# Kernel optimization log

Hardware: AMD Instinct MI355X
Metric: run time of the kernel (lower is better)

Reference implementation:

```python
import jax, jax.numpy as jnp
import numpy as np

T, B, D, H, Q = 512, 256, 128, 128, 8


def _qgate(z, theta):
    """Analytic simulation of the QGate circuit.

    Circuit: start |0..0>, RX(z_j) then trainable RX(theta_j) on each wire j
    (RX(a)RX(b)=RX(a+b)), then a CNOT ring w->(w+1)%Q, then <Z_w> on each wire.
    RX(phi)|0> gives <Z>=cos(phi) and independent wires; the CNOT ring permutes
    computational basis states so bit_w = XOR_{j<=w} a_j for w>=1 and
    bit_0 = XOR_{j>=1} a_j, hence <Z_w> = prod_{j<=w} cos(phi_j) for w>=1 and
    <Z_0> = prod_{j>=1} cos(phi_j). Exact, no 2^Q statevector needed.
    """
    c = jnp.cos(z + theta)                      # (B, Q)
    cp = jnp.cumprod(c, axis=-1)                # (B, Q)
    z0 = jnp.prod(c[:, 1:], axis=-1, keepdims=True)
    return jnp.concatenate([z0, cp[:, 1:]], axis=-1)


def setup_inputs() -> dict:
    key = jax.random.key(0)
    ks = jax.random.split(key, 25)
    inp = {"inputs": jax.random.normal(ks[0], (T, B, D), dtype=jnp.float32)}
    s_in = 1.0 / np.sqrt(D + H)
    s_q = 1.0 / np.sqrt(Q)
    names = ["f", "i", "g", "o"]
    for n, gname in enumerate(names):
        k = ks[1 + 6 * n: 1 + 6 * (n + 1)]
        inp["W" + gname] = jax.random.uniform(k[0], (Q, D + H), jnp.float32, -s_in, s_in)
        inp["b" + gname] = jax.random.uniform(k[1], (Q,), jnp.float32, -s_in, s_in)
        inp["th" + gname] = jax.random.normal(k[2], (Q,), jnp.float32)  # trainable RX angles
        inp["U" + gname] = jax.random.uniform(k[3], (H, Q), jnp.float32, -s_q, s_q)
        inp["c" + gname] = jax.random.uniform(k[4], (H,), jnp.float32, -s_q, s_q)
    return inp


def reference(inputs, Wf, bf, thf, Uf, cf,
              Wi, bi, thi, Ui, ci,
              Wg, bg, thg, Ug, cg,
              Wo, bo, tho, Uo, co):
    bsz = inputs.shape[1]
    hdim = Uf.shape[0]
    h0 = jnp.zeros((bsz, hdim), inputs.dtype)
    c0 = jnp.zeros((bsz, hdim), inputs.dtype)

    def gate(comb, W, b, th, U, cb):
        return _qgate(comb @ W.T + b, th) @ U.T + cb

    def step(carry, x):
        hx, cx = carry
        comb = jnp.concatenate([x, hx], axis=1)          # (B, D+H)
        f = jax.nn.sigmoid(gate(comb, Wf, bf, thf, Uf, cf))
        i = jax.nn.sigmoid(gate(comb, Wi, bi, thi, Ui, ci))
        g = jnp.tanh(gate(comb, Wg, bg, thg, Ug, cg))
        o = jax.nn.sigmoid(gate(comb, Wo, bo, tho, Uo, co))
        cx = f * cx + i * g
        hx = o * jnp.tanh(cx)
        return (hx, cx), hx

    (hx, cx), outs = jax.lax.scan(step, (h0, c0), inputs)
    return outs, hx, cx
```

## Files before the change

### kernel.cpp

```cpp
#include <hip/hip_runtime.h>

#define TT 512
#define BB 256
#define DD 128
#define HH 128
#define QQ 8

struct Params {
    const float* x;
    const float* W[4];
    const float* b[4];
    const float* th[4];
    const float* U[4];
    const float* cb[4];
    float* out;
};

__device__ __forceinline__ float rcp_f(float x)  { return __builtin_amdgcn_rcpf(x); }
__device__ __forceinline__ float exp2_f(float x) { return __builtin_amdgcn_exp2f(x); }

template<int CTRL>
__device__ __forceinline__ float dpp_mov(float x) {
    int r = __builtin_amdgcn_update_dpp(0, __float_as_int(x), CTRL, 0xF, 0xF, true);
    return __int_as_float(r);
}
template<int CTRL, int RM>
__device__ __forceinline__ float dpp_mul1(float x) {
    int r = __builtin_amdgcn_update_dpp(0x3f800000 , __float_as_int(x),
                                        CTRL, RM, 0xF, false);
    return __int_as_float(r);
}
#define RDLANE(v, l) __int_as_float(__builtin_amdgcn_readlane(__float_as_int(v), (l)))

__device__ __forceinline__ void bar_lds() {
    asm volatile("s_waitcnt lgkmcnt(0)\n\ts_barrier" ::: "memory");
}

__global__ __launch_bounds__(256, 1) void qlstm(Params p) {
    __shared__ __align__(16) float xbuf[2][8][144];
    __shared__ __align__(16) float hbuf[144];
    __shared__ float pre[512];
    __shared__ float zxbuf[2][32];

    const int tid = threadIdx.x;
    const int bId = blockIdx.x;
    const int ln  = tid & 63;
    const int wv  = tid >> 6;
    const int qub = ln >> 3;
    const int part8 = ln & 7;

    float Wh[16];
    {
        const float* Wg = p.W[wv] + qub * (DD + HH) + DD + part8 * 16;
        #pragma unroll
        for (int j = 0; j < 16; ++j) Wh[j] = Wg[j];
    }
    const float breg = p.b[wv][qub] + p.th[wv][qub];

    const int gz = 2 * (wv - 2) + (ln >> 5);
    const int qz = (ln >> 2) & 7;
    const int pz = ln & 3;
    float Wx[32];
    if (wv >= 2) {
        const float* Wg = p.W[gz] + qz * (DD + HH) + pz * 32;
        #pragma unroll
        for (int j = 0; j < 32; ++j) Wx[j] = Wg[j];
    }

    const float esc = (wv == 2) ? 2.885390081777927f : -1.442695040888963f;
    float Ua[8], Ub[8];
    #pragma unroll
    for (int j = 0; j < 8; ++j) {
        Ua[j] = p.U[wv][ln * QQ + j] * esc;
        Ub[j] = p.U[wv][(ln + 64) * QQ + j] * esc;
    }
    const float cba = p.cb[wv][ln] * esc;
    const float cbb = p.cb[wv][ln + 64] * esc;

    float cst = 0.f;
    float hn_last = 0.f;

    if (tid < 128) hbuf[tid + 4 * (tid >> 5)] = 0.f;

    const int xc_col  = (ln & 31) * 4;
    const int xc_half = ln >> 5;
    const int xc_slot = xc_col + 4 * (xc_col >> 5);
    float4 xr[4];
    #pragma unroll
    for (int j = 0; j < 4; ++j) xr[j] = make_float4(0.f, 0.f, 0.f, 0.f);

    if (wv == 3) {
        #pragma unroll
        for (int j = 0; j < 4; ++j) {
            const int row = 2 * j + xc_half;
            float4 v = *(const float4*)(p.x + ((size_t)row * BB + bId) * DD + xc_col);
            *(float4*)&xbuf[0][row][xc_slot] = v;
        }
    }
    __syncthreads();

    if (wv >= 2) {
        const float* xrow = &xbuf[0][0][36 * pz];
        float b0 = 0.f, b1 = 0.f, b2 = 0.f, b3 = 0.f;
        #pragma unroll
        for (int i = 0; i < 8; ++i) {
            float4 c4 = *(const float4*)(xrow + 4 * i);
            b0 = fmaf(Wx[4*i+0], c4.x, b0);
            b1 = fmaf(Wx[4*i+1], c4.y, b1);
            b2 = fmaf(Wx[4*i+2], c4.z, b2);
            b3 = fmaf(Wx[4*i+3], c4.w, b3);
        }
        float zx2 = (b0 + b1) + (b2 + b3);
        zx2 += dpp_mov<0xB1>(zx2);
        zx2 += dpp_mov<0x4E>(zx2);
        if ((ln & 3) == 0) zxbuf[0][8 * gz + qz] = zx2;
    }
    __syncthreads();

    const float* hsrc = &hbuf[16 * part8 + 4 * (part8 >> 1)];
    const size_t orow_step = (size_t)BB * HH;
    size_t orow = (size_t)bId * HH + tid;

    #pragma unroll 8
    for (int t = 0; t < TT; ++t) {
        const float zxs = zxbuf[t & 1][8 * wv + qub];
        const float4 h0 = ((const float4*)hsrc)[0];
        const float4 h1 = *(const float4*)(hsrc + 4);
        const float4 h2 = *(const float4*)(hsrc + 8);
        const float4 h3 = *(const float4*)(hsrc + 12);

        if (((t & 7) == 0) && wv == 3) {
            const int tch = (t >> 3) + 1;
            if (tch < TT / 8) {
                #pragma unroll
                for (int j = 0; j < 4; ++j) {
                    const int row = tch * 8 + 2 * j + xc_half;
                    xr[j] = *(const float4*)(p.x + ((size_t)row * BB + bId) * DD + xc_col);
                }
            }
        }

        float a0 = Wh[0] * h0.x, a1 = Wh[1] * h0.y, a2 = Wh[2] * h0.z, a3 = Wh[3] * h0.w;
        a0 = fmaf(Wh[4],  h1.x, a0); a1 = fmaf(Wh[5],  h1.y, a1);
        a2 = fmaf(Wh[6],  h1.z, a2); a3 = fmaf(Wh[7],  h1.w, a3);
        a0 = fmaf(Wh[8],  h2.x, a0); a1 = fmaf(Wh[9],  h2.y, a1);
        a2 = fmaf(Wh[10], h2.z, a2); a3 = fmaf(Wh[11], h2.w, a3);
        a0 = fmaf(Wh[12], h3.x, a0); a1 = fmaf(Wh[13], h3.y, a1);
        a2 = fmaf(Wh[14], h3.z, a2); a3 = fmaf(Wh[15], h3.w, a3);
        float acc = (a0 + a1) + (a2 + a3);
        acc += dpp_mov<0xB1>(acc);
        acc += dpp_mov<0x4E>(acc);
        acc += dpp_mov<0x141>(acc);
        acc += zxs + breg;

        const float cv = __cosf(acc);
        float v = cv;
        v *= dpp_mul1<0x118, 0xF>(v);
        v *= dpp_mul1<0x142, 0xA>(v);
        v *= dpp_mul1<0x143, 0xC>(v);
        float u = (ln < 8) ? 1.f : cv;
        u *= dpp_mul1<0x118, 0xF>(u);
        u *= dpp_mul1<0x142, 0xA>(u);
        u *= dpp_mul1<0x143, 0xC>(u);
        const float q0 = RDLANE(u, 63);
        const float q1 = RDLANE(v, 8);
        const float q2 = RDLANE(v, 16);
        const float q3 = RDLANE(v, 24);
        const float q4 = RDLANE(v, 32);
        const float q5 = RDLANE(v, 40);
        const float q6 = RDLANE(v, 48);
        const float q7 = RDLANE(v, 56);

        float a01 = fmaf(Ua[1], q1, Ua[0] * q0);
        float b01 = fmaf(Ub[1], q1, Ub[0] * q0);
        float a23 = fmaf(Ua[3], q3, Ua[2] * q2);
        float b23 = fmaf(Ub[3], q3, Ub[2] * q2);
        float a45 = fmaf(Ua[5], q5, Ua[4] * q4);
        float b45 = fmaf(Ub[5], q5, Ub[4] * q4);
        float a67 = fmaf(Ua[7], q7, Ua[6] * q6);
        float b67 = fmaf(Ub[7], q7, Ub[6] * q6);
        float pa = ((a01 + a23) + (a45 + a67)) + cba;
        float pb = ((b01 + b23) + (b45 + b67)) + cbb;
        pre[wv * 128 + ln]      = pa;
        pre[wv * 128 + 64 + ln] = pb;

        bar_lds();

        if (tid < 128) {
            float p_f = (wv == 0) ? pa : pre[tid];
            float p_i = (wv == 1) ? pb : pre[128 + tid];
            float p_g = pre[256 + tid];
            float p_o = pre[384 + tid];
            float fg = rcp_f(1.f + exp2_f(p_f));
            float ig = rcp_f(1.f + exp2_f(p_i));
            float gg = fmaf(-2.f, rcp_f(1.f + exp2_f(p_g)), 1.f);
            float og = rcp_f(1.f + exp2_f(p_o));
            cst = fmaf(fg, cst, ig * gg);
            float tc = fmaf(-2.f, rcp_f(1.f + exp2_f(cst * 2.885390081777927f)), 1.f);
            float hn = og * tc;
            hn_last = hn;
            hbuf[tid + 4 * (tid >> 5)] = hn;
            p.out[orow] = hn;
            orow += orow_step;
        } else {
            if (wv == 3 && (t & 7) == 6) {
                const int tch = (t >> 3) + 1;
                if (tch < TT / 8) {
                    #pragma unroll
                    for (int j = 0; j < 4; ++j) {
                        const int row = 2 * j + xc_half;
                        *(float4*)&xbuf[tch & 1][row][xc_slot] = xr[j];
                    }
                }
            }
            if (t < TT - 1) {
                const int tn = t + 1;
                const float* xrow = &xbuf[(tn >> 3) & 1][tn & 7][36 * pz];
                float4 c[8];
                #pragma unroll
                for (int i = 0; i < 8; ++i) c[i] = *(const float4*)(xrow + 4 * i);
                float b0 = Wx[0] * c[0].x, b1 = Wx[1] * c[0].y;
                float b2 = Wx[2] * c[0].z, b3 = Wx[3] * c[0].w;
                #pragma unroll
                for (int i = 1; i < 8; ++i) {
                    b0 = fmaf(Wx[4*i+0], c[i].x, b0);
                    b1 = fmaf(Wx[4*i+1], c[i].y, b1);
                    b2 = fmaf(Wx[4*i+2], c[i].z, b2);
                    b3 = fmaf(Wx[4*i+3], c[i].w, b3);
                }
                float zx2 = (b0 + b1) + (b2 + b3);
                zx2 += dpp_mov<0xB1>(zx2);
                zx2 += dpp_mov<0x4E>(zx2);
                if ((ln & 3) == 0) zxbuf[tn & 1][8 * gz + qz] = zx2;
            }
        }
        bar_lds();
    }

    if (tid < 128) {
        p.out[(size_t)TT * BB * HH + (size_t)bId * HH + tid] = hn_last;
        p.out[(size_t)TT * BB * HH + (size_t)BB * HH + (size_t)bId * HH + tid] = cst;
    }
}

extern "C" void kernel_launch(void* const* d_in, const int* in_sizes, int n_in,
                              void* d_out, int out_size, void* d_ws, size_t ws_size,
                              hipStream_t stream) {
    (void)in_sizes; (void)n_in; (void)out_size; (void)d_ws; (void)ws_size;
    Params p;
    p.x = (const float*)d_in[0];
    for (int g = 0; g < 4; ++g) {
        p.W[g]  = (const float*)d_in[1 + 5 * g + 0];
        p.b[g]  = (const float*)d_in[1 + 5 * g + 1];
        p.th[g] = (const float*)d_in[1 + 5 * g + 2];
        p.U[g]  = (const float*)d_in[1 + 5 * g + 3];
        p.cb[g] = (const float*)d_in[1 + 5 * g + 4];
    }
    p.out = (float*)d_out;
    hipLaunchKernelGGL(qlstm, dim3(BB), dim3(256), 0, stream, p);
}
```

Baseline: 362.0 us.

## Precompute input projection in separate GEMM kernel, stream zx into recurrent loop

Splits the input-to-gate projection (x @ W_x) out of the sequential recurrence into a separate fully parallel kernel that writes a T×B×32 workspace. The recurrent kernel then loads only the precomputed 32 projections per timestep, double-buffered in LDS in chunks of 8 steps, instead of staging and reducing 128-wide x rows every step. This shortens the serial per-step critical path, but adds a second launch and a 16MB workspace round-trip through HBM. The old kernel is kept as a fallback for when no workspace is available.

```diff
diff --git a/kernel.cpp b/kernel.cpp
--- a/kernel.cpp
+++ b/kernel.cpp
@@ -13,7 +13,14 @@
     const float* th[4];
     const float* U[4];
     const float* cb[4];
+    const float* zx;
     float* out;
+};
+
+struct GParams {
+    const float* x;
+    const float* W[4];
+    float* zx;
 };
 
 __device__ __forceinline__ float rcp_f(float x)  { return __builtin_amdgcn_rcpf(x); }
@@ -36,7 +43,184 @@
     asm volatile("s_waitcnt lgkmcnt(0)\n\ts_barrier" ::: "memory");
 }
 
+__global__ __launch_bounds__(256, 1) void zxgemm(GParams g) {
+    const int tid = threadIdx.x;
+    const int l   = tid & 63;
+    const int wv  = tid >> 6;
+    const int gw  = blockIdx.x * 4 + wv;
+    const int t   = gw >> 3;
+    const int b0  = (gw & 7) * 32;
+    const int gq  = l >> 1;
+    const int half = l & 1;
+
+    const float* Wp = g.W[gq >> 3] + (gq & 7) * (DD + HH) + half * 64;
+    float4 w4[16];
+    #pragma unroll
+    for (int j = 0; j < 16; ++j) w4[j] = *(const float4*)(Wp + 4 * j);
+
+    float* zrow = g.zx + ((size_t)t * BB + b0) * 32 + gq;
+    const float* xbase = g.x + ((size_t)t * BB + b0) * DD + half * 64;
+
+    for (int bb = 0; bb < 32; ++bb) {
+        const float* xp = xbase + (size_t)bb * DD;
+        float a0 = 0.f, a1 = 0.f, a2 = 0.f, a3 = 0.f;
+        #pragma unroll
+        for (int j = 0; j < 16; ++j) {
+            float4 v = *(const float4*)(xp + 4 * j);
+            a0 = fmaf(w4[j].x, v.x, a0);
+            a1 = fmaf(w4[j].y, v.y, a1);
+            a2 = fmaf(w4[j].z, v.z, a2);
+            a3 = fmaf(w4[j].w, v.w, a3);
+        }
+        float s = (a0 + a1) + (a2 + a3);
+        s += dpp_mov<0xB1>(s);
+        if (half == 0) zrow[(size_t)bb * 32] = s;
+    }
+}
+
 __global__ __launch_bounds__(256, 1) void qlstm(Params p) {
+    __shared__ __align__(16) float hbuf[144];
+    __shared__ float pre[512];
+    __shared__ __align__(16) float zxw[2][8][32];
+
+    const int tid = threadIdx.x;
+    const int bId = blockIdx.x;
+    const int ln  = tid & 63;
+    const int wv  = tid >> 6;
+    const int qub = ln >> 3;
+    const int part8 = ln & 7;
+
+    float Wh[16];
+    {
+        const float* Wg = p.W[wv] + qub * (DD + HH) + DD + part8 * 16;
+        #pragma unroll
+        for (int j = 0; j < 16; ++j) Wh[j] = Wg[j];
+    }
+    const float breg = p.b[wv][qub] + p.th[wv][qub];
+
+    const float esc = (wv == 2) ? 2.885390081777927f : -1.442695040888963f;
+    float Ua[8], Ub[8];
+    #pragma unroll
+    for (int j = 0; j < 8; ++j) {
+        Ua[j] = p.U[wv][ln * QQ + j] * esc;
+        Ub[j] = p.U[wv][(ln + 64) * QQ + j] * esc;
+    }
+    const float cba = p.cb[wv][ln] * esc;
+    const float cbb = p.cb[wv][ln + 64] * esc;
+
+    float cst = 0.f;
+    float hn_last = 0.f;
+
+    if (tid < 128) hbuf[tid + 4 * (tid >> 5)] = 0.f;
+
+    const int zst = ln >> 3;
+    const int zc  = (ln & 7) * 4;
+    float4 zr = make_float4(0.f, 0.f, 0.f, 0.f);
+    if (wv == 2) {
+        float4 v = *(const float4*)(p.zx + ((size_t)zst * BB + bId) * 32 + zc);
+        *(float4*)&zxw[0][zst][zc] = v;
+    }
+    __syncthreads();
+
+    const float* hsrc = &hbuf[16 * part8 + 4 * (part8 >> 1)];
+    const size_t orow_step = (size_t)BB * HH;
+    size_t orow = (size_t)bId * HH + tid;
+
+    #pragma unroll 8
+    for (int t = 0; t < TT; ++t) {
+        const float zxs = zxw[(t >> 3) & 1][t & 7][8 * wv + qub];
+        const float4 h0 = ((const float4*)hsrc)[0];
+        const float4 h1 = *(const float4*)(hsrc + 4);
+        const float4 h2 = *(const float4*)(hsrc + 8);
+        const float4 h3 = *(const float4*)(hsrc + 12);
+
+        float a0 = Wh[0] * h0.x, a1 = Wh[1] * h0.y, a2 = Wh[2] * h0.z, a3 = Wh[3] * h0.w;
+        a0 = fmaf(Wh[4],  h1.x, a0); a1 = fmaf(Wh[5],  h1.y, a1);
+        a2 = fmaf(Wh[6],  h1.z, a2); a3 = fmaf(Wh[7],  h1.w, a3);
+        a0 = fmaf(Wh[8],  h2.x, a0); a1 = fmaf(Wh[9],  h2.y, a1);
+        a2 = fmaf(Wh[10], h2.z, a2); a3 = fmaf(Wh[11], h2.w, a3);
+        a0 = fmaf(Wh[12], h3.x, a0); a1 = fmaf(Wh[13], h3.y, a1);
+        a2 = fmaf(Wh[14], h3.z, a2); a3 = fmaf(Wh[15], h3.w, a3);
+        float acc = (a0 + a1) + (a2 + a3);
+        acc += dpp_mov<0xB1>(acc);
+        acc += dpp_mov<0x4E>(acc);
+        acc += dpp_mov<0x141>(acc);
+        acc += zxs + breg;
+
+        const float cv = __cosf(acc);
+        float v = cv;
+        v *= dpp_mul1<0x118, 0xF>(v);
+        v *= dpp_mul1<0x142, 0xA>(v);
+        v *= dpp_mul1<0x143, 0xC>(v);
+        float u = (ln < 8) ? 1.f : cv;
+        u *= dpp_mul1<0x118, 0xF>(u);
+        u *= dpp_mul1<0x142, 0xA>(u);
+        u *= dpp_mul1<0x143, 0xC>(u);
+        const float q0 = RDLANE(u, 63);
+        const float q1 = RDLANE(v, 8);
+        const float q2 = RDLANE(v, 16);
+        const float q3 = RDLANE(v, 24);
+        const float q4 = RDLANE(v, 32);
+        const float q5 = RDLANE(v, 40);
+        const float q6 = RDLANE(v, 48);
+        const float q7 = RDLANE(v, 56);
+
+        float a01 = fmaf(Ua[1], q1, Ua[0] * q0);
+        float b01 = fmaf(Ub[1], q1, Ub[0] * q0);
+        float a23 = fmaf(Ua[3], q3, Ua[2] * q2);
+        float b23 = fmaf(Ub[3], q3, Ub[2] * q2);
+        float a45 = fmaf(Ua[5], q5, Ua[4] * q4);
+        float b45 = fmaf(Ub[5], q5, Ub[4] * q4);
+        float a67 = fmaf(Ua[7], q7, Ua[6] * q6);
+        float b67 = fmaf(Ub[7], q7, Ub[6] * q6);
+        float pa = ((a01 + a23) + (a45 + a67)) + cba;
+        float pb = ((b01 + b23) + (b45 + b67)) + cbb;
+        pre[wv * 128 + ln]      = pa;
+        pre[wv * 128 + 64 + ln] = pb;
+
+        bar_lds();
+
+        if (tid < 128) {
+            float p_f = (wv == 0) ? pa : pre[tid];
+            float p_i = (wv == 1) ? pb : pre[128 + tid];
+            float p_g = pre[256 + tid];
+            float p_o = pre[384 + tid];
+            float fg = rcp_f(1.f + exp2_f(p_f));
+            float ig = rcp_f(1.f + exp2_f(p_i));
+            float gg = fmaf(-2.f, rcp_f(1.f + exp2_f(p_g)), 1.f);
+            float og = rcp_f(1.f + exp2_f(p_o));
+            cst = fmaf(fg, cst, ig * gg);
+            float tc = fmaf(-2.f, rcp_f(1.f + exp2_f(cst * 2.885390081777927f)), 1.f);
+            float hn = og * tc;
+            hn_last = hn;
+            hbuf[tid + 4 * (tid >> 5)] = hn;
+            p.out[orow] = hn;
+            orow += orow_step;
+        } else if (wv == 2) {
+            if ((t & 7) == 0) {
+                const int tch = (t >> 3) + 1;
+                if (tch < TT / 8) {
+                    const int s = tch * 8 + zst;
+                    zr = *(const float4*)(p.zx + ((size_t)s * BB + bId) * 32 + zc);
+                }
+            }
+            if ((t & 7) == 6) {
+                const int tch = (t >> 3) + 1;
+                if (tch < TT / 8) {
+                    *(float4*)&zxw[tch & 1][zst][zc] = zr;
+                }
+            }
+        }
+        bar_lds();
+    }
+
+    if (tid < 128) {
+        p.out[(size_t)TT * BB * HH + (size_t)bId * HH + tid] = hn_last;
+        p.out[(size_t)TT * BB * HH + (size_t)BB * HH + (size_t)bId * HH + tid] = cst;
+    }
+}
+
+__global__ __launch_bounds__(256, 1) void qlstm_fb(Params p) {
     __shared__ __align__(16) float xbuf[2][8][144];
     __shared__ __align__(16) float hbuf[144];
     __shared__ float pre[512];
@@ -246,7 +430,7 @@
 extern "C" void kernel_launch(void* const* d_in, const int* in_sizes, int n_in,
                               void* d_out, int out_size, void* d_ws, size_t ws_size,
                               hipStream_t stream) {
-    (void)in_sizes; (void)n_in; (void)out_size; (void)d_ws; (void)ws_size;
+    (void)in_sizes; (void)n_in; (void)out_size;
     Params p;
     p.x = (const float*)d_in[0];
     for (int g = 0; g < 4; ++g) {
@@ -257,5 +441,18 @@
         p.cb[g] = (const float*)d_in[1 + 5 * g + 4];
     }
     p.out = (float*)d_out;
-    hipLaunchKernelGGL(qlstm, dim3(BB), dim3(256), 0, stream, p);
-}
+
+    const size_t ZXB = (size_t)TT * BB * 32 * sizeof(float);
+    if (d_ws != nullptr && ws_size >= ZXB) {
+        GParams g;
+        g.x = p.x;
+        for (int i = 0; i < 4; ++i) g.W[i] = p.W[i];
+        g.zx = (float*)d_ws;
+        p.zx = (const float*)d_ws;
+        hipLaunchKernelGGL(zxgemm, dim3(TT * BB / 32 / 4), dim3(256), 0, stream, g);
+        hipLaunchKernelGGL(qlstm, dim3(BB), dim3(256), 0, stream, p);
+    } else {
+        p.zx = nullptr;
+        hipLaunchKernelGGL(qlstm_fb, dim3(BB), dim3(256), 0, stream, p);
+    }
+}
```

New measurement: 480.4 us. 1.33x slower.

## Add producer waves that precompute input projections ahead of the recurrence

Applied to the files above, without the earlier changes.

The block grows to 512 threads. Four extra producer waves compute the x·W input projection (plus bias and theta) for future timesteps straight from global memory and write it into a full-sequence LDS table, running ahead of the recurrent waves. The recurrent waves no longer do any x-side work; they read the precomputed value and use the hardware cos on a fract of an argument pre-scaled by 1/2π. This removes x-projection work from the serial critical path. In exchange it adds a 64KB LDS table, and the wider block adds more waves to every per-step barrier.

```diff
diff --git a/kernel.cpp b/kernel.cpp
--- a/kernel.cpp
+++ b/kernel.cpp
@@ -5,6 +5,7 @@
 #define DD 128
 #define HH 128
 #define QQ 8
+#define INV2PI 0.15915494309189535f
 
 struct Params {
     const float* x;
@@ -36,11 +37,10 @@
     asm volatile("s_waitcnt lgkmcnt(0)\n\ts_barrier" ::: "memory");
 }
 
-__global__ __launch_bounds__(256, 1) void qlstm(Params p) {
-    __shared__ __align__(16) float xbuf[2][8][144];
+__global__ __launch_bounds__(512, 1) void qlstm(Params p) {
+    __shared__ __align__(16) float zxr[TT][32];
     __shared__ __align__(16) float hbuf[144];
     __shared__ float pre[512];
-    __shared__ float zxbuf[2][32];
 
     const int tid = threadIdx.x;
     const int bId = blockIdx.x;
@@ -50,139 +50,146 @@
     const int part8 = ln & 7;
 
     float Wh[16];
-    {
+    float Ua[8], Ub[8], cba = 0.f, cbb = 0.f;
+    float4 wx[16], xr[16];
+    float bb = 0.f;
+    int tp = 0, pgq = 0, phalf = 0;
+    const float* xb = nullptr;
+
+    if (wv < 4) {
         const float* Wg = p.W[wv] + qub * (DD + HH) + DD + part8 * 16;
         #pragma unroll
-        for (int j = 0; j < 16; ++j) Wh[j] = Wg[j];
-    }
-    const float breg = p.b[wv][qub] + p.th[wv][qub];
-
-    const int gz = 2 * (wv - 2) + (ln >> 5);
-    const int qz = (ln >> 2) & 7;
-    const int pz = ln & 3;
-    float Wx[32];
-    if (wv >= 2) {
-        const float* Wg = p.W[gz] + qz * (DD + HH) + pz * 32;
+        for (int j = 0; j < 16; ++j) Wh[j] = Wg[j] * INV2PI;
+        const float esc = (wv == 2) ? 2.885390081777927f : -1.442695040888963f;
         #pragma unroll
-        for (int j = 0; j < 32; ++j) Wx[j] = Wg[j];
-    }
-
-    const float esc = (wv == 2) ? 2.885390081777927f : -1.442695040888963f;
-    float Ua[8], Ub[8];
-    #pragma unroll
-    for (int j = 0; j < 8; ++j) {
-        Ua[j] = p.U[wv][ln * QQ + j] * esc;
-        Ub[j] = p.U[wv][(ln + 64) * QQ + j] * esc;
-    }
-    const float cba = p.cb[wv][ln] * esc;
-    const float cbb = p.cb[wv][ln + 64] * esc;
-
-    float cst = 0.f;
-    float hn_last = 0.f;
-
-    if (tid < 128) hbuf[tid + 4 * (tid >> 5)] = 0.f;
-
-    const int xc_col  = (ln & 31) * 4;
-    const int xc_half = ln >> 5;
-    const int xc_slot = xc_col + 4 * (xc_col >> 5);
-    float4 xr[4];
-    #pragma unroll
-    for (int j = 0; j < 4; ++j) xr[j] = make_float4(0.f, 0.f, 0.f, 0.f);
-
-    if (wv == 3) {
+        for (int j = 0; j < 8; ++j) {
+            Ua[j] = p.U[wv][ln * QQ + j] * esc;
+            Ub[j] = p.U[wv][(ln + 64) * QQ + j] * esc;
+        }
+        cba = p.cb[wv][ln] * esc;
+        cbb = p.cb[wv][ln + 64] * esc;
+        if (tid < 128) hbuf[tid + 4 * (tid >> 5)] = 0.f;
+    } else {
+        pgq   = ln >> 1;
+        phalf = ln & 1;
+        const float* Wp = p.W[pgq >> 3] + (pgq & 7) * (DD + HH) + phalf * 64;
         #pragma unroll
-        for (int j = 0; j < 4; ++j) {
-            const int row = 2 * j + xc_half;
-            float4 v = *(const float4*)(p.x + ((size_t)row * BB + bId) * DD + xc_col);
-            *(float4*)&xbuf[0][row][xc_slot] = v;
-        }
-    }
-    __syncthreads();
-
-    if (wv >= 2) {
-        const float* xrow = &xbuf[0][0][36 * pz];
-        float b0 = 0.f, b1 = 0.f, b2 = 0.f, b3 = 0.f;
-        #pragma unroll
-        for (int i = 0; i < 8; ++i) {
-            float4 c4 = *(const float4*)(xrow + 4 * i);
-            b0 = fmaf(Wx[4*i+0], c4.x, b0);
-            b1 = fmaf(Wx[4*i+1], c4.y, b1);
-            b2 = fmaf(Wx[4*i+2], c4.z, b2);
-            b3 = fmaf(Wx[4*i+3], c4.w, b3);
-        }
-        float zx2 = (b0 + b1) + (b2 + b3);
-        zx2 += dpp_mov<0xB1>(zx2);
-        zx2 += dpp_mov<0x4E>(zx2);
-        if ((ln & 3) == 0) zxbuf[0][8 * gz + qz] = zx2;
-    }
-    __syncthreads();
+        for (int j = 0; j < 16; ++j) {
+            float4 w = *(const float4*)(Wp + 4 * j);
+            wx[j] = make_float4(w.x * INV2PI, w.y * INV2PI,
+                                w.z * INV2PI, w.w * INV2PI);
+        }
+        bb = (p.b[pgq >> 3][pgq & 7] + p.th[pgq >> 3][pgq & 7]) * INV2PI;
+        xb = p.x + (size_t)bId * DD + phalf * 64;
+        tp = wv - 4;
+        {
+            const float* xp = xb + (size_t)tp * (BB * DD);
+            #pragma unroll
+            for (int j = 0; j < 16; ++j) xr[j] = *(const float4*)(xp + 4 * j);
+        }
+        for (int i = 0; i < 16; ++i) {
+            float b0 = wx[0].x * xr[0].x, b1 = wx[0].y * xr[0].y;
+            float b2 = wx[0].z * xr[0].z, b3 = wx[0].w * xr[0].w;
+            #pragma unroll
+            for (int j = 1; j < 16; ++j) {
+                b0 = fmaf(wx[j].x, xr[j].x, b0); b1 = fmaf(wx[j].y, xr[j].y, b1);
+                b2 = fmaf(wx[j].z, xr[j].z, b2); b3 = fmaf(wx[j].w, xr[j].w, b3);
+            }
+            float s = (b0 + b1) + (b2 + b3);
+            s += dpp_mov<0xB1>(s);
+            if (phalf == 0) zxr[tp][pgq] = s + bb;
+            tp += 4;
+            if (tp < TT) {
+                const float* xp = xb + (size_t)tp * (BB * DD);
+                #pragma unroll
+                for (int j = 0; j < 16; ++j) xr[j] = *(const float4*)(xp + 4 * j);
+            }
+        }
+    }
+
+    bar_lds();
 
     const float* hsrc = &hbuf[16 * part8 + 4 * (part8 >> 1)];
-    const size_t orow_step = (size_t)BB * HH;
+    const size_t ostep = (size_t)BB * HH;
     size_t orow = (size_t)bId * HH + tid;
+    float cst = 0.f, hn_last = 0.f;
 
     #pragma unroll 8
     for (int t = 0; t < TT; ++t) {
-        const float zxs = zxbuf[t & 1][8 * wv + qub];
-        const float4 h0 = ((const float4*)hsrc)[0];
-        const float4 h1 = *(const float4*)(hsrc + 4);
-        const float4 h2 = *(const float4*)(hsrc + 8);
-        const float4 h3 = *(const float4*)(hsrc + 12);
-
-        if (((t & 7) == 0) && wv == 3) {
-            const int tch = (t >> 3) + 1;
-            if (tch < TT / 8) {
+        float pa, pb;
+        if (wv < 4) {
+            const float zxv = zxr[t][8 * wv + qub];
+            const float4 h0 = *(const float4*)(hsrc);
+            const float4 h1 = *(const float4*)(hsrc + 4);
+            const float4 h2 = *(const float4*)(hsrc + 8);
+            const float4 h3 = *(const float4*)(hsrc + 12);
+
+            float a0 = Wh[0] * h0.x, a1 = Wh[1] * h0.y;
+            float a2 = Wh[2] * h0.z, a3 = Wh[3] * h0.w;
+            a0 = fmaf(Wh[4],  h1.x, a0); a1 = fmaf(Wh[5],  h1.y, a1);
+            a2 = fmaf(Wh[6],  h1.z, a2); a3 = fmaf(Wh[7],  h1.w, a3);
+            a0 = fmaf(Wh[8],  h2.x, a0); a1 = fmaf(Wh[9],  h2.y, a1);
+            a2 = fmaf(Wh[10], h2.z, a2); a3 = fmaf(Wh[11], h2.w, a3);
+            a0 = fmaf(Wh[12], h3.x, a0); a1 = fmaf(Wh[13], h3.y, a1);
+            a2 = fmaf(Wh[14], h3.z, a2); a3 = fmaf(Wh[15], h3.w, a3);
+            float acc = (a0 + a1) + (a2 + a3);
+            acc += dpp_mov<0xB1>(acc);
+            acc += dpp_mov<0x4E>(acc);
+            acc += dpp_mov<0x141>(acc);
+            acc += zxv;
+
+            const float cv = __builtin_amdgcn_cosf(__builtin_amdgcn_fractf(acc));
+            float v = cv;
+            v *= dpp_mul1<0x118, 0xF>(v);
+            v *= dpp_mul1<0x142, 0xA>(v);
+            v *= dpp_mul1<0x143, 0xC>(v);
+            float u = (ln < 8) ? 1.f : cv;
+            u *= dpp_mul1<0x118, 0xF>(u);
+            u *= dpp_mul1<0x142, 0xA>(u);
+            u *= dpp_mul1<0x143, 0xC>(u);
+            const float q0 = RDLANE(u, 63);
+            const float q1 = RDLANE(v, 8);
+            const float q2 = RDLANE(v, 16);
+            const float q3 = RDLANE(v, 24);
+            const float q4 = RDLANE(v, 32);
+            const float q5 = RDLANE(v, 40);
+            const float q6 = RDLANE(v, 48);
+            const float q7 = RDLANE(v, 56);
+
+            float a01 = fmaf(Ua[1], q1, Ua[0] * q0);
+            float b01 = fmaf(Ub[1], q1, Ub[0] * q0);
+            float a23 = fmaf(Ua[3], q3, Ua[2] * q2);
+            float b23 = fmaf(Ub[3], q3, Ub[2] * q2);
+            float a45 = fmaf(Ua[5], q5, Ua[4] * q4);
+            float b45 = fmaf(Ub[5], q5, Ub[4] * q4);
+            float a67 = fmaf(Ua[7], q7, Ua[6] * q6);
+            float b67 = fmaf(Ub[7], q7, Ub[6] * q6);
+            pa = ((a01 + a23) + (a45 + a67)) + cba;
+            pb = ((b01 + b23) + (b45 + b67)) + cbb;
+            pre[wv * 128 + ln]      = pa;
+            pre[wv * 128 + 64 + ln] = pb;
+        } else {
+            if (tp < TT) {
+                float b0 = wx[0].x * xr[0].x, b1 = wx[0].y * xr[0].y;
+                float b2 = wx[0].z * xr[0].z, b3 = wx[0].w * xr[0].w;
                 #pragma unroll
-                for (int j = 0; j < 4; ++j) {
-                    const int row = tch * 8 + 2 * j + xc_half;
-                    xr[j] = *(const float4*)(p.x + ((size_t)row * BB + bId) * DD + xc_col);
+                for (int j = 1; j < 16; ++j) {
+                    b0 = fmaf(wx[j].x, xr[j].x, b0);
+                    b1 = fmaf(wx[j].y, xr[j].y, b1);
+                    b2 = fmaf(wx[j].z, xr[j].z, b2);
+                    b3 = fmaf(wx[j].w, xr[j].w, b3);
+                }
+                float s = (b0 + b1) + (b2 + b3);
+                s += dpp_mov<0xB1>(s);
+                if (phalf == 0) zxr[tp][pgq] = s + bb;
+                tp += 4;
+                if (tp < TT) {
+                    const float* xp = xb + (size_t)tp * (BB * DD);
+                    #pragma unroll
+                    for (int j = 0; j < 16; ++j) xr[j] = *(const float4*)(xp + 4 * j);
                 }
             }
         }
-
-        float a0 = Wh[0] * h0.x, a1 = Wh[1] * h0.y, a2 = Wh[2] * h0.z, a3 = Wh[3] * h0.w;
-        a0 = fmaf(Wh[4],  h1.x, a0); a1 = fmaf(Wh[5],  h1.y, a1);
-        a2 = fmaf(Wh[6],  h1.z, a2); a3 = fmaf(Wh[7],  h1.w, a3);
-        a0 = fmaf(Wh[8],  h2.x, a0); a1 = fmaf(Wh[9],  h2.y, a1);
-        a2 = fmaf(Wh[10], h2.z, a2); a3 = fmaf(Wh[11], h2.w, a3);
-        a0 = fmaf(Wh[12], h3.x, a0); a1 = fmaf(Wh[13], h3.y, a1);
-        a2 = fmaf(Wh[14], h3.z, a2); a3 = fmaf(Wh[15], h3.w, a3);
-        float acc = (a0 + a1) + (a2 + a3);
-        acc += dpp_mov<0xB1>(acc);
-        acc += dpp_mov<0x4E>(acc);
-        acc += dpp_mov<0x141>(acc);
-        acc += zxs + breg;
-
-        const float cv = __cosf(acc);
-        float v = cv;
-        v *= dpp_mul1<0x118, 0xF>(v);
-        v *= dpp_mul1<0x142, 0xA>(v);
-        v *= dpp_mul1<0x143, 0xC>(v);
-        float u = (ln < 8) ? 1.f : cv;
-        u *= dpp_mul1<0x118, 0xF>(u);
-        u *= dpp_mul1<0x142, 0xA>(u);
-        u *= dpp_mul1<0x143, 0xC>(u);
-        const float q0 = RDLANE(u, 63);
-        const float q1 = RDLANE(v, 8);
-        const float q2 = RDLANE(v, 16);
-        const float q3 = RDLANE(v, 24);
-        const float q4 = RDLANE(v, 32);
-        const float q5 = RDLANE(v, 40);
-        const float q6 = RDLANE(v, 48);
-        const float q7 = RDLANE(v, 56);
-
-        float a01 = fmaf(Ua[1], q1, Ua[0] * q0);
-        float b01 = fmaf(Ub[1], q1, Ub[0] * q0);
-        float a23 = fmaf(Ua[3], q3, Ua[2] * q2);
-        float b23 = fmaf(Ub[3], q3, Ub[2] * q2);
-        float a45 = fmaf(Ua[5], q5, Ua[4] * q4);
-        float b45 = fmaf(Ub[5], q5, Ub[4] * q4);
-        float a67 = fmaf(Ua[7], q7, Ua[6] * q6);
-        float b67 = fmaf(Ub[7], q7, Ub[6] * q6);
-        float pa = ((a01 + a23) + (a45 + a67)) + cba;
-        float pb = ((b01 + b23) + (b45 + b67)) + cbb;
-        pre[wv * 128 + ln]      = pa;
-        pre[wv * 128 + 64 + ln] = pb;
 
         bar_lds();
 
@@ -201,38 +208,7 @@
             hn_last = hn;
             hbuf[tid + 4 * (tid >> 5)] = hn;
             p.out[orow] = hn;
-            orow += orow_step;
-        } else {
-            if (wv == 3 && (t & 7) == 6) {
-                const int tch = (t >> 3) + 1;
-                if (tch < TT / 8) {
-                    #pragma unroll
-                    for (int j = 0; j < 4; ++j) {
-                        const int row = 2 * j + xc_half;
-                        *(float4*)&xbuf[tch & 1][row][xc_slot] = xr[j];
-                    }
-                }
-            }
-            if (t < TT - 1) {
-                const int tn = t + 1;
-                const float* xrow = &xbuf[(tn >> 3) & 1][tn & 7][36 * pz];
-                float4 c[8];
-                #pragma unroll
-                for (int i = 0; i < 8; ++i) c[i] = *(const float4*)(xrow + 4 * i);
-                float b0 = Wx[0] * c[0].x, b1 = Wx[1] * c[0].y;
-                float b2 = Wx[2] * c[0].z, b3 = Wx[3] * c[0].w;
-                #pragma unroll
-                for (int i = 1; i < 8; ++i) {
-                    b0 = fmaf(Wx[4*i+0], c[i].x, b0);
-                    b1 = fmaf(Wx[4*i+1], c[i].y, b1);
-                    b2 = fmaf(Wx[4*i+2], c[i].z, b2);
-                    b3 = fmaf(Wx[4*i+3], c[i].w, b3);
-                }
-                float zx2 = (b0 + b1) + (b2 + b3);
-                zx2 += dpp_mov<0xB1>(zx2);
-                zx2 += dpp_mov<0x4E>(zx2);
-                if ((ln & 3) == 0) zxbuf[tn & 1][8 * gz + qz] = zx2;
-            }
+            orow += ostep;
         }
         bar_lds();
     }
@@ -257,5 +233,5 @@
         p.cb[g] = (const float*)d_in[1 + 5 * g + 4];
     }
     p.out = (float*)d_out;
-    hipLaunchKernelGGL(qlstm, dim3(BB), dim3(256), 0, stream, p);
-}
+    hipLaunchKernelGGL(qlstm, dim3(BB), dim3(512), 0, stream, p);
+}
```

Measured after the change: 434.6 us. 1.2x slower.
